# Kernel optimization log

Measured on AMD Instinct MI355X. Metric: run time of the kernel, lower is better.

The kernel has to match this reference:

```python
import jax, jax.numpy as jnp
import numpy as np


def setup_inputs() -> dict:
    key = jax.random.key(0)
    k1, k2 = jax.random.split(key)
    B, C, F = 8192, 10000, 2048
    x = jax.random.normal(k1, (B, F), dtype=jnp.float32)
    means = jax.random.normal(k2, (C, F), dtype=jnp.float32)
    return {"x": x, "means": means}


def reference(x, means):
    # Negative squared Euclidean distance from each sample to each class mean.
    # Same math as sum((x[:,None,:]-means[None,:,:])**2, -1), expressed via the
    x_sq = jnp.sum(x * x, axis=-1, keepdims=True)          # [B, 1]
    m_sq = jnp.sum(means * means, axis=-1)                  # [C]
    cross = jnp.einsum("bf,cf->bc", x, means)              # [B, C] GEMM
    dist_sq = x_sq + m_sq[None, :] - 2.0 * cross            # [B, C]
    return -dist_sq
```

## Files before the change

kernel.cpp:

```cpp
#include <hip/hip_runtime.h>
#include <hip/hip_bf16.h>
#include <stdint.h>

#define BDIM 8192
#define CDIM 10000
#define CPAD 10240
#define FDIM 2048

#define BM 256
#define BN 256
#define BKB 64
#define NT (FDIM / BKB)
#define NI (NT / 2)
#define TM (BDIM / BM)
#define TN (CPAD / BN)
#define NWG (TM * TN)

#define HT_BYTES   8192
#define DBUF_BYTES 32768
#define EPI_WAVE_BYTES 4352
#define LDS_BYTES  65536

#define QSF   (6.5f / 127.0f)
#define INVQ  (127.0f / 6.5f)
#define TSC   (2.0f * QSF * QSF)

typedef __attribute__((ext_vector_type(4))) int   i32x4;
typedef __attribute__((ext_vector_type(4))) float f32x4;

#define AS1 __attribute__((address_space(1)))
#define AS3 __attribute__((address_space(3)))

__global__ __launch_bounds__(256) void convert_rows(
    const float* __restrict__ xsrc, const float* __restrict__ msrc,
    signed char* __restrict__ Xq, signed char* __restrict__ Mq,
    float* __restrict__ xsq, float* __restrict__ msq)
{
    const int b = blockIdx.x;
    const int tid = threadIdx.x;

    const float* src;
    signed char* drow;
    float* sq;
    int row;
    if (b < BDIM) {
        row = b; src = xsrc + (size_t)row * FDIM;
        drow = Xq + (size_t)row * FDIM; sq = xsq + row;
    } else {
        row = b - BDIM;
        drow = Mq + (size_t)row * FDIM; sq = msq + row;
        if (row >= CDIM) {
            ((uint2*)drow)[tid] = make_uint2(0, 0);
            if (tid == 0) *sq = 0.0f;
            return;
        }
        src = msrc + (size_t)row * FDIM;
    }

    const float4* s = (const float4*)src;
    float4 v0 = s[tid * 2 + 0];
    float4 v1 = s[tid * 2 + 1];

    float f[8] = {v0.x, v0.y, v0.z, v0.w, v1.x, v1.y, v1.z, v1.w};
    float ssum = 0.0f;
    union { unsigned char u[8]; uint2 v; } pk;
#pragma unroll
    for (int j = 0; j < 8; ++j) {
        ssum += f[j] * f[j];
        int q = (int)__builtin_rintf(f[j] * INVQ);
        q = q > 127 ? 127 : (q < -127 ? -127 : q);
        pk.u[j] = (unsigned char)(q & 0xff);
    }
    ((uint2*)drow)[tid] = pk.v;

#pragma unroll
    for (int off = 32; off > 0; off >>= 1)
        ssum += __shfl_down(ssum, off, 64);
    __shared__ float red[4];
    if ((tid & 63) == 0) red[tid >> 6] = ssum;
    __syncthreads();
    if (tid == 0) *sq = red[0] + red[1] + red[2] + red[3];
}

#define MIDSYNC() do { \
    __builtin_amdgcn_s_barrier(); \
    asm volatile("s_waitcnt lgkmcnt(0)" ::: "memory"); \
    __builtin_amdgcn_sched_barrier(0); \
} while (0)

#define ENDBAR() do { \
    __builtin_amdgcn_s_barrier(); \
    __builtin_amdgcn_sched_barrier(0); \
} while (0)

#define SCHEDBAR() __builtin_amdgcn_sched_barrier(0)

#define QUAD(MH, AV, BV, NH) do { \
    __builtin_amdgcn_s_setprio(1); \
    _Pragma("unroll") \
    for (int f = 0; f < 4; ++f) \
      _Pragma("unroll") \
      for (int f2 = 0; f2 < 2; ++f2) \
        acc[(MH)*4+f][(NH)*2+f2] = __builtin_amdgcn_mfma_i32_16x16x64_i8( \
            AV[f], BV[f2], acc[(MH)*4+f][(NH)*2+f2], 0, 0, 0); \
    __builtin_amdgcn_s_setprio(0); \
} while (0)

__global__ __launch_bounds__(512, 2) void nscm_gemm(
    const signed char* __restrict__ Xq, const signed char* __restrict__ Mq,
    const float* __restrict__ xsq, const float* __restrict__ msq,
    float* __restrict__ out)
{
    extern __shared__ char lds[];

    const int tid  = threadIdx.x;
    const int lane = tid & 63;
    const int wave = tid >> 6;
    const int wr = wave >> 2;
    const int wc = wave & 3;
    const int fr = lane & 15;
    const int kq = lane >> 4;

    const int bid = blockIdx.x;
    const int xcd = bid & 7;
    const int c   = bid >> 3;
    const int sub = c >> 5;
    const int tile_m = xcd * 4 + (c & 3);
    const int tile_n = sub * 8 + ((c >> 2) & 7);
    const int row0 = tile_m * BM;
    const int col0 = tile_n * BN;

    const int sw  = tid >> 2;
    const int sce = (((tid & 3) ^ ((tid >> 3) & 3))) * 16;
    const int rslot = (kq ^ ((fr >> 1) & 3)) * 16;

    i32x4 acc[8][4] = {};
    i32x4 av0[4], av1[4], bv0[2], bv1[2];

    auto stageA = [&](int kt, int buf, int h) {
        const int grow = row0 + (sw >> 6) * 128 + h * 64 + (sw & 63);
        const signed char* src = Xq + (size_t)grow * FDIM + kt * BKB + sce;
        char* dst = lds + buf * DBUF_BYTES + h * HT_BYTES + wave * 1024;
        __builtin_amdgcn_global_load_lds((const AS1 void*)src,
                                         (AS3 void*)dst, 16, 0, 0);
    };
    auto stageB = [&](int kt, int buf, int h) {
        const int grow = col0 + (sw >> 5) * 64 + h * 32 + (sw & 31);
        const signed char* src = Mq + (size_t)grow * FDIM + kt * BKB + sce;
        char* dst = lds + buf * DBUF_BYTES + 16384 + h * HT_BYTES + wave * 1024;
        __builtin_amdgcn_global_load_lds((const AS1 void*)src,
                                         (AS3 void*)dst, 16, 0, 0);
    };

    auto loadA = [&](int buf, int mh, i32x4 (&dst)[4]) {
        const char* base = lds + buf * DBUF_BYTES + mh * HT_BYTES;
#pragma unroll
        for (int f = 0; f < 4; ++f) {
            const int w = wr * 64 + f * 16 + fr;
            dst[f] = *(const i32x4*)(base + w * 64 + rslot);
        }
    };
    auto loadB = [&](int buf, int nh, i32x4 (&dst)[2]) {
        const char* base = lds + buf * DBUF_BYTES + 16384 + nh * HT_BYTES;
#pragma unroll
        for (int f = 0; f < 2; ++f) {
            const int w = wc * 32 + f * 16 + fr;
            dst[f] = *(const i32x4*)(base + w * 64 + rslot);
        }
    };

    stageA(0, 0, 0); stageB(0, 0, 0); stageB(0, 0, 1); stageA(0, 0, 1);
    stageA(1, 1, 0); stageB(1, 1, 0); stageB(1, 1, 1);
    asm volatile("s_waitcnt vmcnt(3)" ::: "memory");
    __builtin_amdgcn_s_barrier();
    SCHEDBAR();
    loadA(0, 0, av0); loadB(0, 0, bv0);
    SCHEDBAR();

    for (int t = 0; t < NI; ++t) {
        const int kO1 = 2 * t + 1;
        const int kE2 = (2 * t + 2) & (NT - 1);
        const int kO3 = (2 * t + 3) & (NT - 1);

        stageA(kO1, 1, 1);
        MIDSYNC();
        loadB(0, 1, bv1);
        SCHEDBAR();
        QUAD(0, av0, bv0, 0);
        ENDBAR();

        stageA(kE2, 0, 0);
        MIDSYNC();
        loadA(0, 1, av1);
        SCHEDBAR();
        QUAD(0, av0, bv1, 1);
        ENDBAR();

        stageB(kE2, 0, 0);
        MIDSYNC();
        QUAD(1, av1, bv0, 0);
        ENDBAR();

        stageB(kE2, 0, 1);
        asm volatile("s_waitcnt vmcnt(3)" ::: "memory");
        MIDSYNC();
        loadA(1, 0, av0); loadB(1, 0, bv0);
        SCHEDBAR();
        QUAD(1, av1, bv1, 1);
        ENDBAR();

        stageA(kE2, 0, 1);
        MIDSYNC();
        loadB(1, 1, bv1);
        SCHEDBAR();
        QUAD(0, av0, bv0, 0);
        ENDBAR();

        stageA(kO3, 1, 0);
        MIDSYNC();
        loadA(1, 1, av1);
        SCHEDBAR();
        QUAD(0, av0, bv1, 1);
        ENDBAR();

        stageB(kO3, 1, 0);
        MIDSYNC();
        QUAD(1, av1, bv0, 0);
        ENDBAR();

        stageB(kO3, 1, 1);
        asm volatile("s_waitcnt vmcnt(3)" ::: "memory");
        MIDSYNC();
        loadA(0, 0, av0); loadB(0, 0, bv0);
        SCHEDBAR();
        QUAD(1, av1, bv1, 1);
        ENDBAR();
    }

    asm volatile("s_waitcnt vmcnt(0) lgkmcnt(0)" ::: "memory");
    __builtin_amdgcn_s_barrier();
    SCHEDBAR();

    float* wtile = (float*)(lds + wave * EPI_WAVE_BYTES);
    const int rr = lane >> 4;
    const int cq = lane & 15;
    const int gc = col0 + wc * 64 + cq * 4;
    float ms0 = 0.f, ms1 = 0.f, ms2 = 0.f, ms3 = 0.f;
    if (gc < CDIM) {
        ms0 = msq[gc]; ms1 = msq[gc + 1]; ms2 = msq[gc + 2]; ms3 = msq[gc + 3];
    }

#pragma unroll
    for (int p = 0; p < 8; ++p) {
#pragma unroll
        for (int fn = 0; fn < 4; ++fn) {
            const int lr = kq * 4;
            const int lc = fn * 16 + fr;
#pragma unroll
            for (int r = 0; r < 4; ++r)
                wtile[(lr + r) * 68 + lc] = (float)acc[p][fn][r];
        }
        asm volatile("s_waitcnt lgkmcnt(0)" ::: "memory");
        SCHEDBAR();

        if (gc < CDIM) {
#pragma unroll
            for (int i = 0; i < 4; ++i) {
                const int row = i * 4 + rr;
                f32x4 v = *(const f32x4*)&wtile[row * 68 + cq * 4];
                const int gr = row0 + wr * 128 + p * 16 + row;
                const float xsv = xsq[gr];
                f32x4 o;
                o[0] = TSC * v[0] - xsv - ms0;
                o[1] = TSC * v[1] - xsv - ms1;
                o[2] = TSC * v[2] - xsv - ms2;
                o[3] = TSC * v[3] - xsv - ms3;
                __builtin_nontemporal_store(
                    o, (f32x4*)(out + (size_t)gr * CDIM + gc));
            }
        }
        asm volatile("s_waitcnt lgkmcnt(0)" ::: "memory");
        SCHEDBAR();
    }
}

extern "C" void kernel_launch(void* const* d_in, const int* in_sizes, int n_in,
                              void* d_out, int out_size, void* d_ws, size_t ws_size,
                              hipStream_t stream) {
    const float* x     = (const float*)d_in[0];
    const float* means = (const float*)d_in[1];
    float* out = (float*)d_out;

    char* ws = (char*)d_ws;
    signed char* Xq = (signed char*)ws;
    signed char* Mq = (signed char*)(ws + (size_t)BDIM * FDIM);
    float* xsq = (float*)(ws + (size_t)BDIM * FDIM + (size_t)CPAD * FDIM);
    float* msq = xsq + BDIM;

    (void)hipFuncSetAttribute((const void*)nscm_gemm,
                              hipFuncAttributeMaxDynamicSharedMemorySize,
                              LDS_BYTES);

    convert_rows<<<BDIM + CPAD, 256, 0, stream>>>(x, means, Xq, Mq, xsq, msq);

    nscm_gemm<<<NWG, 512, LDS_BYTES, stream>>>(Xq, Mq, xsq, msq, out);
}
```

Measured before the change: 213.9 us.

## Restructure int8 GEMM main loop into four phases of sixteen MFMAs

Cuts the ping-pong main loop from eight barrier-separated phases of eight MFMAs to four phases of sixteen MFMAs. Each phase now issues two global-to-LDS stage loads, and both B halves are preloaded into registers for each k-tile. The goal is half as many barriers and waitcnt points per k-step, so more MFMA work sits between synchronisations. The cost is extra register pressure from the doubled B fragments and a changed vmcnt wait depth, which could limit occupancy or expose load latency.

After: 223.1 us. +4.3%, slower.

```diff
diff --git a/kernel.cpp b/kernel.cpp
--- a/kernel.cpp
+++ b/kernel.cpp
@@ -95,14 +95,16 @@
 
 #define SCHEDBAR() __builtin_amdgcn_sched_barrier(0)
 
-#define QUAD(MH, AV, BV, NH) do { \
+#define QUAD16(MH, AV, BV) do { \
     __builtin_amdgcn_s_setprio(1); \
     _Pragma("unroll") \
-    for (int f = 0; f < 4; ++f) \
+    for (int nh = 0; nh < 2; ++nh) \
       _Pragma("unroll") \
-      for (int f2 = 0; f2 < 2; ++f2) \
-        acc[(MH)*4+f][(NH)*2+f2] = __builtin_amdgcn_mfma_i32_16x16x64_i8( \
-            AV[f], BV[f2], acc[(MH)*4+f][(NH)*2+f2], 0, 0, 0); \
+      for (int f = 0; f < 4; ++f) \
+        _Pragma("unroll") \
+        for (int f2 = 0; f2 < 2; ++f2) \
+          acc[(MH)*4+f][nh*2+f2] = __builtin_amdgcn_mfma_i32_16x16x64_i8( \
+              AV[f], BV[nh][f2], acc[(MH)*4+f][nh*2+f2], 0, 0, 0); \
     __builtin_amdgcn_s_setprio(0); \
 } while (0)
 
@@ -135,7 +137,7 @@
     const int rslot = (kq ^ ((fr >> 1) & 3)) * 16;
 
     i32x4 acc[8][4] = {};
-    i32x4 av0[4], av1[4], bv0[2], bv1[2];
+    i32x4 avA[4], avB[4], bv0[2][2], bv1[2][2];
 
     auto stageA = [&](int kt, int buf, int h) {
         const int grow = row0 + (sw >> 6) * 128 + h * 64 + (sw & 63);
@@ -169,12 +171,12 @@
         }
     };
 
-    stageA(0, 0, 0); stageB(0, 0, 0); stageB(0, 0, 1); stageA(0, 0, 1);
-    stageA(1, 1, 0); stageB(1, 1, 0); stageB(1, 1, 1);
-    asm volatile("s_waitcnt vmcnt(3)" ::: "memory");
+    stageA(0, 0, 0); stageB(0, 0, 0); stageA(0, 0, 1); stageB(0, 0, 1);
+    stageA(1, 1, 0); stageB(1, 1, 0);
+    asm volatile("s_waitcnt vmcnt(2)" ::: "memory");
     __builtin_amdgcn_s_barrier();
     SCHEDBAR();
-    loadA(0, 0, av0); loadB(0, 0, bv0);
+    loadA(0, 0, avA); loadB(0, 0, bv0[0]); loadB(0, 1, bv0[1]);
     SCHEDBAR();
 
     for (int t = 0; t < NI; ++t) {
@@ -183,57 +185,37 @@
         const int kO3 = (2 * t + 3) & (NT - 1);
 
         stageA(kO1, 1, 1);
-        MIDSYNC();
-        loadB(0, 1, bv1);
-        SCHEDBAR();
-        QUAD(0, av0, bv0, 0);
+        stageB(kO1, 1, 1);
+        MIDSYNC();
+        loadA(0, 1, avB);
+        SCHEDBAR();
+        QUAD16(0, avA, bv0);
         ENDBAR();
 
         stageA(kE2, 0, 0);
-        MIDSYNC();
-        loadA(0, 1, av1);
-        SCHEDBAR();
-        QUAD(0, av0, bv1, 1);
-        ENDBAR();
-
         stageB(kE2, 0, 0);
-        MIDSYNC();
-        QUAD(1, av1, bv0, 0);
-        ENDBAR();
-
+        asm volatile("s_waitcnt vmcnt(2)" ::: "memory");
+        MIDSYNC();
+        loadA(1, 0, avA); loadB(1, 0, bv1[0]); loadB(1, 1, bv1[1]);
+        SCHEDBAR();
+        QUAD16(1, avB, bv0);
+        ENDBAR();
+
+        stageA(kE2, 0, 1);
         stageB(kE2, 0, 1);
-        asm volatile("s_waitcnt vmcnt(3)" ::: "memory");
-        MIDSYNC();
-        loadA(1, 0, av0); loadB(1, 0, bv0);
-        SCHEDBAR();
-        QUAD(1, av1, bv1, 1);
-        ENDBAR();
-
-        stageA(kE2, 0, 1);
-        MIDSYNC();
-        loadB(1, 1, bv1);
-        SCHEDBAR();
-        QUAD(0, av0, bv0, 0);
+        MIDSYNC();
+        loadA(1, 1, avB);
+        SCHEDBAR();
+        QUAD16(0, avA, bv1);
         ENDBAR();
 
         stageA(kO3, 1, 0);
-        MIDSYNC();
-        loadA(1, 1, av1);
-        SCHEDBAR();
-        QUAD(0, av0, bv1, 1);
-        ENDBAR();
-
         stageB(kO3, 1, 0);
-        MIDSYNC();
-        QUAD(1, av1, bv0, 0);
-        ENDBAR();
-
-        stageB(kO3, 1, 1);
-        asm volatile("s_waitcnt vmcnt(3)" ::: "memory");
-        MIDSYNC();
-        loadA(0, 0, av0); loadB(0, 0, bv0);
-        SCHEDBAR();
-        QUAD(1, av1, bv1, 1);
+        asm volatile("s_waitcnt vmcnt(2)" ::: "memory");
+        MIDSYNC();
+        loadA(0, 0, avA); loadB(0, 0, bv0[0]); loadB(0, 1, bv0[1]);
+        SCHEDBAR();
+        QUAD16(1, avB, bv1);
         ENDBAR();
     }
 
```
